# Kernel optimization log

Hardware: AMD Instinct MI355X
Metric: run time of the kernel (lower is better)

## Reference

```python
import jax, jax.numpy as jnp
import numpy as np

N_NODES = 50000
N_EDGES = 800000
F_IN = 16
HEADS = 4
CONV_DIMS = [(16, 16), (16, 32), (32, 32), (32, 32), (32, 32), (32, 64)]
LIN_DIMS = [(128, 256), (256, 64), (64, 16), (16, 1)]


def setup_inputs() -> dict:
    key = jax.random.key(0)
    ks = iter(jax.random.split(key, 64))
    inp = {}
    inp["x"] = jax.random.normal(next(ks), (N_NODES, F_IN), dtype=jnp.float32)
    inp["edge_index"] = jax.random.randint(next(ks), (2, N_EDGES), 0, N_NODES, dtype=jnp.int32)
    for i, (ci, co) in enumerate(CONV_DIMS, 1):
        inp[f"W{i}"] = jax.random.normal(next(ks), (ci, HEADS * co), dtype=jnp.float32) * (1.0 / np.sqrt(ci))
        inp[f"U{i}"] = jax.random.normal(next(ks), (ci, HEADS), dtype=jnp.float32) * (1.0 / np.sqrt(ci))
        inp[f"c{i}"] = jnp.zeros((HEADS,), jnp.float32)
        inp[f"b{i}"] = jnp.zeros((co,), jnp.float32)
    for i, d in zip((1, 2, 3), (32, 32, 64)):
        inp[f"g{i}"] = jnp.ones((d,), jnp.float32)
        inp[f"be{i}"] = jnp.zeros((d,), jnp.float32)
    for name, (ci, co) in zip(("1", "2", "3", "o"), LIN_DIMS):
        inp[f"lw{name}"] = jax.random.normal(next(ks), (ci, co), dtype=jnp.float32) * (1.0 / np.sqrt(ci))
        inp[f"lb{name}"] = jnp.zeros((co,), jnp.float32)
    return inp


def _feast(x, src, dst, W, U, c, b):
    # FeaStConv (PyG): q = softmax_h(U^T (x_j - x_i) + c); out_i = mean_j sum_h q_h * (W_h x_j) + b
    n = x.shape[0]
    out_ch = W.shape[1] // HEADS
    q = jax.nn.softmax((x[src] - x[dst]) @ U + c, axis=-1)            # [E, H]
    xw = (x @ W).reshape(n, HEADS, out_ch)                            # [N, H, O]
    msg = jnp.einsum('eho,eh->eo', xw[src], q)                        # [E, O]
    s = jax.ops.segment_sum(msg, dst, num_segments=n)
    cnt = jax.ops.segment_sum(jnp.ones((src.shape[0], 1), msg.dtype), dst, num_segments=n)
    return s / jnp.maximum(cnt, 1.0) + b


def _bn(x, g, b, eps=1e-5):
    # training-mode BatchNorm over the node dimension
    m = x.mean(0)
    v = x.var(0)
    return (x - m) * jax.lax.rsqrt(v + eps) * g + b


def _forward(x, edge_index, convs, bns, lins):
    # FeaStConv adds self-loops by default
    loops = jnp.arange(x.shape[0], dtype=edge_index.dtype)
    src = jnp.concatenate([edge_index[0], loops])
    dst = jnp.concatenate([edge_index[1], loops])
    h = jax.nn.relu(_feast(x, src, dst, *convs[0]))
    x1 = _bn(jax.nn.relu(_feast(h, src, dst, *convs[1])), *bns[0])
    x2 = jax.nn.relu(_feast(x1, src, dst, *convs[2]))
    x2 = _bn(jax.nn.relu(_feast(x2, src, dst, *convs[3])), *bns[1])
    x3 = jax.nn.relu(_feast(x2, src, dst, *convs[4]))
    x3 = _bn(jax.nn.relu(_feast(x3, src, dst, *convs[5])), *bns[2])
    z = jax.nn.relu(jnp.concatenate([x1, x2, x3], axis=1))            # [N, 128]
    (lw1, lb1), (lw2, lb2), (lw3, lb3), (lwo, lbo) = lins
    z = jax.nn.relu(z @ lw1 + lb1)
    z = jax.nn.relu(z @ lw2 + lb2)
    z = jax.nn.relu(z @ lw3 + lb3)
    return jax.nn.sigmoid(z @ lwo + lbo)                              # [N, 1]


def reference(x, edge_index, W1, U1, c1, b1, W2, U2, c2, b2, W3, U3, c3, b3, W4, U4, c4, b4, W5, U5, c5, b5, W6, U6, c6, b6, g1, be1, g2, be2, g3, be3, lw1, lb1, lw2, lb2, lw3, lb3, lwo, lbo):
    convs = [(W1, U1, c1, b1), (W2, U2, c2, b2), (W3, U3, c3, b3), (W4, U4, c4, b4), (W5, U5, c5, b5), (W6, U6, c6, b6)]
    bns = [(g1, be1), (g2, be2), (g3, be3)]
    lins = [(lw1, lb1), (lw2, lb2), (lw3, lb3), (lwo, lbo)]
    return _forward(x, edge_index, convs, bns, lins)
```

## Files before the change

kernel.cpp:

```cpp
#include <hip/hip_runtime.h>

constexpr int NN = 50000;
constexpr int NE = 800000;
constexpr int SNB = (NN + 255) / 256;

typedef _Float16 h8 __attribute__((ext_vector_type(8)));
typedef _Float16 h4v __attribute__((ext_vector_type(4)));
typedef float f32x4 __attribute__((ext_vector_type(4)));

__global__ void hist_kernel(const int* __restrict__ dst, int* __restrict__ deg) {
    int e = blockIdx.x * blockDim.x + threadIdx.x;
    if (e < NE) atomicAdd(&deg[dst[e]], 1);
}

__global__ __launch_bounds__(256) void scan_bsum_kernel(const int* __restrict__ deg,
                                                        int* __restrict__ bsum) {
    int i = blockIdx.x * 256 + threadIdx.x;
    int v = (i < NN) ? deg[i] : 0;
#pragma unroll
    for (int off = 32; off > 0; off >>= 1) v += __shfl_xor(v, off);
    __shared__ int ws[4];
    if ((threadIdx.x & 63) == 0) ws[threadIdx.x >> 6] = v;
    __syncthreads();
    if (threadIdx.x == 0) bsum[blockIdx.x] = ws[0] + ws[1] + ws[2] + ws[3];
}

__global__ __launch_bounds__(256) void scan_tops_kernel(const int* __restrict__ bsum,
                                                        int* __restrict__ bpre) {
    int tid = threadIdx.x;
    int v = (tid < SNB) ? bsum[tid] : 0;
    int lane = tid & 63, wid = tid >> 6;
    int x = v;
#pragma unroll
    for (int off = 1; off < 64; off <<= 1) {
        int y = __shfl_up(x, off, 64);
        if (lane >= off) x += y;
    }
    __shared__ int wsum[4];
    if (lane == 63) wsum[wid] = x;
    __syncthreads();
    int wpre = 0;
    for (int w = 0; w < wid; w++) wpre += wsum[w];
    if (tid < SNB) bpre[tid] = wpre + x - v;
    if (tid == 0) bpre[SNB] = wsum[0] + wsum[1] + wsum[2] + wsum[3];
}

__global__ __launch_bounds__(256) void scan_final_kernel(const int* __restrict__ deg,
                                                         const int* __restrict__ bpre,
                                                         int* __restrict__ row_ptr,
                                                         int* __restrict__ fillc) {
    int i = blockIdx.x * 256 + threadIdx.x;
    int v = (i < NN) ? deg[i] : 0;
    int lane = threadIdx.x & 63, wid = threadIdx.x >> 6;
    int x = v;
#pragma unroll
    for (int off = 1; off < 64; off <<= 1) {
        int y = __shfl_up(x, off, 64);
        if (lane >= off) x += y;
    }
    __shared__ int wsum[4];
    if (lane == 63) wsum[wid] = x;
    __syncthreads();
    int wpre = 0;
    for (int w = 0; w < wid; w++) wpre += wsum[w];
    int ex = bpre[blockIdx.x] + wpre + x - v;
    if (i < NN) { row_ptr[i] = ex; fillc[i] = ex; }
    if (i == 0) row_ptr[NN] = bpre[SNB];
}

__global__ void fill_kernel(const int* __restrict__ src, const int* __restrict__ dst,
                            int* __restrict__ fillc, int2* __restrict__ col2) {
    int e = blockIdx.x * blockDim.x + threadIdx.x;
    if (e < NE) {
        int d = dst[e];
        int k = atomicAdd(&fillc[d], 1);
        col2[k] = make_int2(src[e], d);
    }
}

template <int CI>
__global__ __launch_bounds__(256) void prep_kernel(const float* __restrict__ x,
                                                   const float* __restrict__ U,
                                                   _Float16* __restrict__ xh,
                                                   float* __restrict__ t) {
    __shared__ float Us[CI * 4];
    for (int i = threadIdx.x; i < CI * 4; i += 256) Us[i] = U[i];
    __syncthreads();
    int n = blockIdx.x * 256 + threadIdx.x;
    if (n >= NN) return;
    float xr[CI];
    const float4* xv = reinterpret_cast<const float4*>(x + (size_t)n * CI);
#pragma unroll
    for (int q = 0; q < CI / 4; q++) {
        float4 v = xv[q];
        xr[4 * q + 0] = v.x; xr[4 * q + 1] = v.y; xr[4 * q + 2] = v.z; xr[4 * q + 3] = v.w;
    }
    h8* xo = reinterpret_cast<h8*>(xh + (size_t)n * CI);
#pragma unroll
    for (int q = 0; q < CI / 8; q++) {
        h8 hv;
#pragma unroll
        for (int u = 0; u < 8; u++) hv[u] = (_Float16)xr[8 * q + u];
        xo[q] = hv;
    }
    float a0 = 0.f, a1 = 0.f, a2 = 0.f, a3 = 0.f;
#pragma unroll
    for (int k = 0; k < CI; k++) {
        float xk = xr[k];
        a0 = fmaf(xk, Us[k * 4 + 0], a0); a1 = fmaf(xk, Us[k * 4 + 1], a1);
        a2 = fmaf(xk, Us[k * 4 + 2], a2); a3 = fmaf(xk, Us[k * 4 + 3], a3);
    }
    reinterpret_cast<float4*>(t)[n] = make_float4(a0, a1, a2, a3);
}

template <int CO>
__global__ __launch_bounds__(256) void tU_kernel(const _Float16* __restrict__ xh,
                                                 const float* __restrict__ U,
                                                 float* __restrict__ t) {
    __shared__ float Us[CO * 4];
    for (int i = threadIdx.x; i < CO * 4; i += 256) Us[i] = U[i];
    __syncthreads();
    int n = blockIdx.x * 256 + threadIdx.x;
    if (n >= NN) return;
    const h8* xp = reinterpret_cast<const h8*>(xh + (size_t)n * CO);
    float t0 = 0.f, t1 = 0.f, t2 = 0.f, t3 = 0.f;
#pragma unroll
    for (int q8 = 0; q8 < CO / 8; q8++) {
        h8 v = xp[q8];
#pragma unroll
        for (int u = 0; u < 8; u++) {
            float r = (float)v[u];
            const float* us = &Us[(q8 * 8 + u) * 4];
            t0 = fmaf(r, us[0], t0); t1 = fmaf(r, us[1], t1);
            t2 = fmaf(r, us[2], t2); t3 = fmaf(r, us[3], t3);
        }
    }
    reinterpret_cast<float4*>(t)[n] = make_float4(t0, t1, t2, t3);
}

__global__ __launch_bounds__(256) void edgeq_kernel(const int2* __restrict__ col2,
                                                    const float* __restrict__ t,
                                                    const float* __restrict__ cvec,
                                                    h4v* __restrict__ qbuf) {
    int k = blockIdx.x * 256 + threadIdx.x;
    if (k >= NE) return;
    int2 sd = col2[k];
    float4 ts = reinterpret_cast<const float4*>(t)[sd.x];
    float4 td = reinterpret_cast<const float4*>(t)[sd.y];
    float4 cv = *reinterpret_cast<const float4*>(cvec);
    float d0 = ts.x - td.x + cv.x, d1 = ts.y - td.y + cv.y;
    float d2 = ts.z - td.z + cv.z, d3 = ts.w - td.w + cv.w;
    float mm = fmaxf(fmaxf(d0, d1), fmaxf(d2, d3));
    float q0 = __expf(d0 - mm), q1 = __expf(d1 - mm);
    float q2 = __expf(d2 - mm), q3 = __expf(d3 - mm);
    float is = 1.f / (q0 + q1 + q2 + q3);
    h4v q;
    q[0] = (_Float16)(q0 * is); q[1] = (_Float16)(q1 * is);
    q[2] = (_Float16)(q2 * is); q[3] = (_Float16)(q3 * is);
    qbuf[k] = q;
}

template <int CI>
__global__ __launch_bounds__(256) void aggC_kernel(const _Float16* __restrict__ xh,
                                                   const h4v* __restrict__ qbuf,
                                                   const float* __restrict__ cvec,
                                                   const int* __restrict__ row_ptr,
                                                   const int2* __restrict__ col2,
                                                   _Float16* __restrict__ y) {
    constexpr int SLOTS = 128 / CI;
    __shared__ float part[2][CI * 4];
    int tid = threadIdx.x;
    int half = tid >> 7;
    int lt = tid & 127;
    int n = blockIdx.x * 2 + half;
    int ch = lt & (CI - 1);
    int slot = lt / CI;
    float4 cv = *reinterpret_cast<const float4*>(cvec);
    float a0 = 0.f, a1 = 0.f, a2 = 0.f, a3 = 0.f;
    if (slot == 0) {
        float m = fmaxf(fmaxf(cv.x, cv.y), fmaxf(cv.z, cv.w));
        float s0 = __expf(cv.x - m), s1 = __expf(cv.y - m),
              s2 = __expf(cv.z - m), s3 = __expf(cv.w - m);
        float sinv = 1.f / (s0 + s1 + s2 + s3);
        float xself = (float)xh[(size_t)n * CI + ch];
        a0 = s0 * sinv * xself; a1 = s1 * sinv * xself;
        a2 = s2 * sinv * xself; a3 = s3 * sinv * xself;
    }
    int beg = row_ptr[n], end = row_ptr[n + 1];
#pragma unroll 2
    for (int e = beg + slot; e < end; e += SLOTS) {
        int s = col2[e].x;
        h4v q = qbuf[e];
        float xv = (float)xh[(size_t)s * CI + ch];
        a0 = fmaf((float)q[0], xv, a0); a1 = fmaf((float)q[1], xv, a1);
        a2 = fmaf((float)q[2], xv, a2); a3 = fmaf((float)q[3], xv, a3);
    }
#pragma unroll
    for (int off = 32; off >= CI; off >>= 1) {
        a0 += __shfl_xor(a0, off); a1 += __shfl_xor(a1, off);
        a2 += __shfl_xor(a2, off); a3 += __shfl_xor(a3, off);
    }
    if (lt >= 64 && lt < 64 + CI) {
        part[half][ch * 4 + 0] = a0; part[half][ch * 4 + 1] = a1;
        part[half][ch * 4 + 2] = a2; part[half][ch * 4 + 3] = a3;
    }
    __syncthreads();
    if (lt < CI) {
        a0 += part[half][ch * 4 + 0]; a1 += part[half][ch * 4 + 1];
        a2 += part[half][ch * 4 + 2]; a3 += part[half][ch * 4 + 3];
        float sc = 1.f / (float)(end - beg + 1);
        _Float16* yo = y + (size_t)n * 4 * CI + ch;
        yo[0]      = (_Float16)(a0 * sc);
        yo[CI]     = (_Float16)(a1 * sc);
        yo[2 * CI] = (_Float16)(a2 * sc);
        yo[3 * CI] = (_Float16)(a3 * sc);
    }
}

template <int K, int CO, int COB, bool STACKED, bool OUT16>
__global__ __launch_bounds__(256) void mfma_dense_kernel(const _Float16* __restrict__ A,
                                                         const float* __restrict__ W,
                                                         const float* __restrict__ bias,
                                                         void* __restrict__ outp) {
    constexpr int KS = K / 16;
    constexpr int OT = COB / 16;
    constexpr int CIc = K / 4;
    __shared__ _Float16 Bf[OT * KS * 64 * 4];
    __shared__ float bS[COB];
    int o0 = blockIdx.y * COB;
    for (int idx = threadIdx.x; idx < OT * KS * 64; idx += 256) {
        int lane = idx & 63;
        int ks = (idx >> 6) % KS;
        int ot = idx / (64 * KS);
        int o = o0 + ot * 16 + (lane & 15);
        int kb = ks * 16 + (lane >> 4) * 4;
        h4v v;
#pragma unroll
        for (int j = 0; j < 4; j++) {
            int k = kb + j;
            float wv;
            if constexpr (STACKED) wv = W[(k % CIc) * (4 * CO) + (k / CIc) * CO + o];
            else                   wv = W[k * CO + o];
            v[j] = (_Float16)wv;
        }
        *reinterpret_cast<h4v*>(&Bf[idx * 4]) = v;
    }
    for (int i = threadIdx.x; i < COB; i += 256) bS[i] = bias[o0 + i];
    __syncthreads();
    int wid = threadIdx.x >> 6, lane = threadIdx.x & 63;
    int row_in = lane & 15;
    int kgrp = lane >> 4;
    for (int mt = blockIdx.x * 4 + wid; mt < NN / 16; mt += gridDim.x * 4) {
        int m0 = mt * 16;
        f32x4 acc[OT];
#pragma unroll
        for (int t = 0; t < OT; t++) acc[t] = {0.f, 0.f, 0.f, 0.f};
        const _Float16* Ab = A + (size_t)(m0 + row_in) * K + kgrp * 4;
#pragma unroll
        for (int ks = 0; ks < KS; ks++) {
            h4v af = *reinterpret_cast<const h4v*>(Ab + ks * 16);
#pragma unroll
            for (int t = 0; t < OT; t++) {
                h4v bf = *reinterpret_cast<const h4v*>(&Bf[((t * KS + ks) * 64 + lane) * 4]);
                acc[t] = __builtin_amdgcn_mfma_f32_16x16x16f16(af, bf, acc[t], 0, 0, 0);
            }
        }
        int orow0 = m0 + kgrp * 4;
#pragma unroll
        for (int t = 0; t < OT; t++) {
            int col = o0 + t * 16 + row_in;
            float b = bS[t * 16 + row_in];
#pragma unroll
            for (int i = 0; i < 4; i++) {
                float v = fmaxf(acc[t][i] + b, 0.f);
                if constexpr (OUT16)
                    ((_Float16*)outp)[(size_t)(orow0 + i) * CO + col] = (_Float16)v;
                else
                    ((float*)outp)[(size_t)(orow0 + i) * CO + col] = v;
            }
        }
    }
}

template <int C>
__global__ __launch_bounds__(256) void bn_reduce_kernel(const float* __restrict__ a,
                                                        float* __restrict__ stats) {
    constexpr int R = 256 / C;
    int cidx = threadIdx.x % C;
    int r = threadIdx.x / C;
    float s = 0.f, s2 = 0.f;
    for (int n = blockIdx.x * R + r; n < NN; n += gridDim.x * R) {
        float v = a[(size_t)n * C + cidx];
        s += v; s2 = fmaf(v, v, s2);
    }
    __shared__ float ls[256], ls2[256];
    ls[threadIdx.x] = s; ls2[threadIdx.x] = s2;
    __syncthreads();
    for (int off = 128; off >= C; off >>= 1) {
        if (threadIdx.x < off) {
            ls[threadIdx.x] += ls[threadIdx.x + off];
            ls2[threadIdx.x] += ls2[threadIdx.x + off];
        }
        __syncthreads();
    }
    if (threadIdx.x < C) {
        atomicAdd(&stats[cidx], ls[threadIdx.x]);
        atomicAdd(&stats[C + cidx], ls2[threadIdx.x]);
    }
}

template <int C>
__global__ __launch_bounds__(256) void bn_norm_prep_kernel(const float* __restrict__ a,
                                                           const float* __restrict__ stats,
                                                           const float* __restrict__ g,
                                                           const float* __restrict__ be,
                                                           const float* __restrict__ U,
                                                           _Float16* __restrict__ xh,
                                                           float* __restrict__ t,
                                                           _Float16* __restrict__ zh,
                                                           int zoff) {
    __shared__ float mS[C], sS[C], beS[C], Us[C * 4];
    if (threadIdx.x < C) {
        int c = threadIdx.x;
        float mean = stats[c] * (1.f / NN);
        float var = stats[C + c] * (1.f / NN) - mean * mean;
        mS[c] = mean;
        sS[c] = rsqrtf(fmaxf(var, 0.f) + 1e-5f) * g[c];
        beS[c] = be[c];
    }
    for (int i = threadIdx.x; i < C * 4; i += 256) Us[i] = U[i];
    __syncthreads();
    int n = blockIdx.x * 256 + threadIdx.x;
    if (n >= NN) return;
    const float4* ap = reinterpret_cast<const float4*>(a + (size_t)n * C);
    h8* xo = reinterpret_cast<h8*>(xh + (size_t)n * C);
    h8* zo = reinterpret_cast<h8*>(zh + (size_t)n * 128 + zoff);
    float t0 = 0.f, t1 = 0.f, t2 = 0.f, t3 = 0.f;
#pragma unroll
    for (int q8 = 0; q8 < C / 8; q8++) {
        h8 hv, zv;
#pragma unroll
        for (int q4 = 0; q4 < 2; q4++) {
            int c4 = q8 * 2 + q4;
            float4 v = ap[c4];
            float r0 = (v.x - mS[c4 * 4 + 0]) * sS[c4 * 4 + 0] + beS[c4 * 4 + 0];
            float r1 = (v.y - mS[c4 * 4 + 1]) * sS[c4 * 4 + 1] + beS[c4 * 4 + 1];
            float r2 = (v.z - mS[c4 * 4 + 2]) * sS[c4 * 4 + 2] + beS[c4 * 4 + 2];
            float r3 = (v.w - mS[c4 * 4 + 3]) * sS[c4 * 4 + 3] + beS[c4 * 4 + 3];
            hv[q4 * 4 + 0] = (_Float16)r0; hv[q4 * 4 + 1] = (_Float16)r1;
            hv[q4 * 4 + 2] = (_Float16)r2; hv[q4 * 4 + 3] = (_Float16)r3;
            zv[q4 * 4 + 0] = (_Float16)fmaxf(r0, 0.f); zv[q4 * 4 + 1] = (_Float16)fmaxf(r1, 0.f);
            zv[q4 * 4 + 2] = (_Float16)fmaxf(r2, 0.f); zv[q4 * 4 + 3] = (_Float16)fmaxf(r3, 0.f);
            const float* us;
            us = &Us[(c4 * 4 + 0) * 4];
            t0 = fmaf(r0, us[0], t0); t1 = fmaf(r0, us[1], t1); t2 = fmaf(r0, us[2], t2); t3 = fmaf(r0, us[3], t3);
            us = &Us[(c4 * 4 + 1) * 4];
            t0 = fmaf(r1, us[0], t0); t1 = fmaf(r1, us[1], t1); t2 = fmaf(r1, us[2], t2); t3 = fmaf(r1, us[3], t3);
            us = &Us[(c4 * 4 + 2) * 4];
            t0 = fmaf(r2, us[0], t0); t1 = fmaf(r2, us[1], t1); t2 = fmaf(r2, us[2], t2); t3 = fmaf(r2, us[3], t3);
            us = &Us[(c4 * 4 + 3) * 4];
            t0 = fmaf(r3, us[0], t0); t1 = fmaf(r3, us[1], t1); t2 = fmaf(r3, us[2], t2); t3 = fmaf(r3, us[3], t3);
        }
        xo[q8] = hv;
        zo[q8] = zv;
    }
    reinterpret_cast<float4*>(t)[n] = make_float4(t0, t1, t2, t3);
}

template <int C>
__global__ __launch_bounds__(256) void bn_norm_z_kernel(const float* __restrict__ a,
                                                        const float* __restrict__ stats,
                                                        const float* __restrict__ g,
                                                        const float* __restrict__ be,
                                                        _Float16* __restrict__ zh,
                                                        int zoff) {
    __shared__ float mS[C], sS[C], beS[C];
    if (threadIdx.x < C) {
        int c = threadIdx.x;
        float mean = stats[c] * (1.f / NN);
        float var = stats[C + c] * (1.f / NN) - mean * mean;
        mS[c] = mean;
        sS[c] = rsqrtf(fmaxf(var, 0.f) + 1e-5f) * g[c];
        beS[c] = be[c];
    }
    __syncthreads();
    int n = blockIdx.x * 256 + threadIdx.x;
    if (n >= NN) return;
    const float4* ap = reinterpret_cast<const float4*>(a + (size_t)n * C);
    h8* zo = reinterpret_cast<h8*>(zh + (size_t)n * 128 + zoff);
#pragma unroll
    for (int q8 = 0; q8 < C / 8; q8++) {
        h8 zv;
#pragma unroll
        for (int q4 = 0; q4 < 2; q4++) {
            int c4 = q8 * 2 + q4;
            float4 v = ap[c4];
            zv[q4 * 4 + 0] = (_Float16)fmaxf((v.x - mS[c4 * 4 + 0]) * sS[c4 * 4 + 0] + beS[c4 * 4 + 0], 0.f);
            zv[q4 * 4 + 1] = (_Float16)fmaxf((v.y - mS[c4 * 4 + 1]) * sS[c4 * 4 + 1] + beS[c4 * 4 + 1], 0.f);
            zv[q4 * 4 + 2] = (_Float16)fmaxf((v.z - mS[c4 * 4 + 2]) * sS[c4 * 4 + 2] + beS[c4 * 4 + 2], 0.f);
            zv[q4 * 4 + 3] = (_Float16)fmaxf((v.w - mS[c4 * 4 + 3]) * sS[c4 * 4 + 3] + beS[c4 * 4 + 3], 0.f);
        }
        zo[q8] = zv;
    }
}

__global__ __launch_bounds__(256) void lin3o_kernel(const _Float16* __restrict__ z2,
                                                    const float* __restrict__ lw3,
                                                    const float* __restrict__ lb3,
                                                    const float* __restrict__ lwo,
                                                    const float* __restrict__ lbo,
                                                    float* __restrict__ out) {
    __shared__ float W3s[64 * 16];
    __shared__ float Wos[16];
    __shared__ float b3s[16];
    for (int i = threadIdx.x; i < 64 * 16; i += 256) W3s[i] = lw3[i];
    if (threadIdx.x < 16) { Wos[threadIdx.x] = lwo[threadIdx.x]; b3s[threadIdx.x] = lb3[threadIdx.x]; }
    __syncthreads();
    int n = blockIdx.x * 256 + threadIdx.x;
    if (n >= NN) return;
    float acc[16];
#pragma unroll
    for (int u = 0; u < 16; u++) acc[u] = b3s[u];
    const h8* zp = reinterpret_cast<const h8*>(z2 + (size_t)n * 64);
#pragma unroll
    for (int k8 = 0; k8 < 8; k8++) {
        h8 v = zp[k8];
#pragma unroll
        for (int u = 0; u < 8; u++) {
            float vf = (float)v[u];
            const float* w = &W3s[(k8 * 8 + u) * 16];
#pragma unroll
            for (int o = 0; o < 16; o++) acc[o] = fmaf(vf, w[o], acc[o]);
        }
    }
    float s = lbo[0];
#pragma unroll
    for (int u = 0; u < 16; u++) s = fmaf(fmaxf(acc[u], 0.f), Wos[u], s);
    out[n] = 1.f / (1.f + __expf(-s));
}

extern "C" void kernel_launch(void* const* d_in, const int* in_sizes, int n_in,
                              void* d_out, int out_size, void* d_ws, size_t ws_size,
                              hipStream_t stream) {
    const float* x = (const float*)d_in[0];
    const int* ei = (const int*)d_in[1];
    const int* esrc = ei;
    const int* edst = ei + NE;
    const float* W[6]; const float* U[6]; const float* C[6]; const float* B[6];
    for (int i = 0; i < 6; i++) {
        W[i] = (const float*)d_in[2 + 4 * i];
        U[i] = (const float*)d_in[3 + 4 * i];
        C[i] = (const float*)d_in[4 + 4 * i];
        B[i] = (const float*)d_in[5 + 4 * i];
    }
    const float* g1 = (const float*)d_in[26]; const float* be1 = (const float*)d_in[27];
    const float* g2 = (const float*)d_in[28]; const float* be2 = (const float*)d_in[29];
    const float* g3 = (const float*)d_in[30]; const float* be3 = (const float*)d_in[31];
    const float* lw1 = (const float*)d_in[32]; const float* lb1 = (const float*)d_in[33];
    const float* lw2 = (const float*)d_in[34]; const float* lb2 = (const float*)d_in[35];
    const float* lw3 = (const float*)d_in[36]; const float* lb3 = (const float*)d_in[37];
    const float* lwo = (const float*)d_in[38]; const float* lbo = (const float*)d_in[39];

    char* w = (char*)d_ws;
    size_t o = 0;
    auto take = [&](size_t bytes) -> char* {
        char* p = w + o;
        o = (o + bytes + 255) & ~(size_t)255;
        return p;
    };
    int* deg = (int*)take((size_t)NN * 4);
    float* stats = (float*)take(3 * 256 * 4);
    size_t zero_bytes = o;
    int* fillc = (int*)take((size_t)NN * 4);
    int* row_ptr = (int*)take((size_t)(NN + 1) * 4);
    int* bsum = (int*)take((size_t)(SNB + 1) * 4);
    int* bpre = (int*)take((size_t)(SNB + 1) * 4);
    int2* col2 = (int2*)take((size_t)NE * 8);
    h4v* qbuf = (h4v*)take((size_t)NE * 8);
    float* t = (float*)take((size_t)NN * 4 * 4);
    _Float16* xh = (_Float16*)take((size_t)NN * 32 * 2);
    char* A = take((size_t)NN * 256 * 2);
    _Float16* y = (_Float16*)A;
    _Float16* z1h = (_Float16*)A;
    _Float16* zh = (_Float16*)take((size_t)NN * 128 * 2);
    float* tmp = (float*)take((size_t)NN * 64 * 4);
    _Float16* z2h = (_Float16*)tmp;
    float* st0 = stats, *st1 = stats + 256, *st2 = stats + 512;

    hipMemsetAsync(d_ws, 0, zero_bytes, stream);

    const int EB = (NE + 255) / 256;
    const int NB = (NN + 255) / 256;
    const int GB = 250;

    hist_kernel<<<EB, 256, 0, stream>>>(edst, deg);
    scan_bsum_kernel<<<SNB, 256, 0, stream>>>(deg, bsum);
    scan_tops_kernel<<<1, 256, 0, stream>>>(bsum, bpre);
    scan_final_kernel<<<SNB, 256, 0, stream>>>(deg, bpre, row_ptr, fillc);
    fill_kernel<<<EB, 256, 0, stream>>>(esrc, edst, fillc, col2);

    prep_kernel<16><<<NB, 256, 0, stream>>>(x, U[0], xh, t);
    edgeq_kernel<<<EB, 256, 0, stream>>>(col2, t, C[0], qbuf);
    aggC_kernel<16><<<NN / 2, 256, 0, stream>>>(xh, qbuf, C[0], row_ptr, col2, y);
    mfma_dense_kernel<64, 16, 16, true, true><<<dim3(GB, 1), 256, 0, stream>>>(y, W[0], B[0], xh);
    tU_kernel<16><<<NB, 256, 0, stream>>>(xh, U[1], t);
    edgeq_kernel<<<EB, 256, 0, stream>>>(col2, t, C[1], qbuf);
    aggC_kernel<16><<<NN / 2, 256, 0, stream>>>(xh, qbuf, C[1], row_ptr, col2, y);
    mfma_dense_kernel<64, 32, 32, true, false><<<dim3(GB, 1), 256, 0, stream>>>(y, W[1], B[1], tmp);
    bn_reduce_kernel<32><<<256, 256, 0, stream>>>(tmp, st0);
    bn_norm_prep_kernel<32><<<NB, 256, 0, stream>>>(tmp, st0, g1, be1, U[2], xh, t, zh, 0);
    edgeq_kernel<<<EB, 256, 0, stream>>>(col2, t, C[2], qbuf);
    aggC_kernel<32><<<NN / 2, 256, 0, stream>>>(xh, qbuf, C[2], row_ptr, col2, y);
    mfma_dense_kernel<128, 32, 32, true, true><<<dim3(GB, 1), 256, 0, stream>>>(y, W[2], B[2], xh);
    tU_kernel<32><<<NB, 256, 0, stream>>>(xh, U[3], t);
    edgeq_kernel<<<EB, 256, 0, stream>>>(col2, t, C[3], qbuf);
    aggC_kernel<32><<<NN / 2, 256, 0, stream>>>(xh, qbuf, C[3], row_ptr, col2, y);
    mfma_dense_kernel<128, 32, 32, true, false><<<dim3(GB, 1), 256, 0, stream>>>(y, W[3], B[3], tmp);
    bn_reduce_kernel<32><<<256, 256, 0, stream>>>(tmp, st1);
    bn_norm_prep_kernel<32><<<NB, 256, 0, stream>>>(tmp, st1, g2, be2, U[4], xh, t, zh, 32);
    edgeq_kernel<<<EB, 256, 0, stream>>>(col2, t, C[4], qbuf);
    aggC_kernel<32><<<NN / 2, 256, 0, stream>>>(xh, qbuf, C[4], row_ptr, col2, y);
    mfma_dense_kernel<128, 32, 32, true, true><<<dim3(GB, 1), 256, 0, stream>>>(y, W[4], B[4], xh);
    tU_kernel<32><<<NB, 256, 0, stream>>>(xh, U[5], t);
    edgeq_kernel<<<EB, 256, 0, stream>>>(col2, t, C[5], qbuf);
    aggC_kernel<32><<<NN / 2, 256, 0, stream>>>(xh, qbuf, C[5], row_ptr, col2, y);
    mfma_dense_kernel<128, 64, 64, true, false><<<dim3(GB, 1), 256, 0, stream>>>(y, W[5], B[5], tmp);
    bn_reduce_kernel<64><<<256, 256, 0, stream>>>(tmp, st2);
    bn_norm_z_kernel<64><<<NB, 256, 0, stream>>>(tmp, st2, g3, be3, zh, 64);

    mfma_dense_kernel<128, 256, 64, false, true><<<dim3(GB, 4), 256, 0, stream>>>(zh, lw1, lb1, z1h);
    mfma_dense_kernel<256, 64, 64, false, true><<<dim3(GB, 1), 256, 0, stream>>>(z1h, lw2, lb2, z2h);
    lin3o_kernel<<<NB, 256, 0, stream>>>(z2h, lw3, lb3, lwo, lbo, (float*)d_out);
}
```

Before: 653.0 us.

## Fuse U-projection into dense epilogue and make edge softmax CSR node-parallel

Removes the separate tU kernel by computing the per-node head projection t = relu(xW+b)·U inside the MFMA dense kernel epilogue, using a 16-lane shuffle reduction. The edge softmax kernel now walks CSR rows with 16 lanes per node, so the destination's t is loaded once and the edge list only stores source indices (int instead of int2). This halves the column array traffic for both edgeq and aggregation, and the aggregation loop unroll goes from 2 to 4. In exchange the dense epilogue does extra shuffles and register work, and the per-node edge loop may leave lanes idle on low-degree nodes.

```diff
diff --git a/kernel.cpp b/kernel.cpp
--- a/kernel.cpp
+++ b/kernel.cpp
@@ -69,12 +69,12 @@
 }
 
 __global__ void fill_kernel(const int* __restrict__ src, const int* __restrict__ dst,
-                            int* __restrict__ fillc, int2* __restrict__ col2) {
+                            int* __restrict__ fillc, int* __restrict__ col) {
     int e = blockIdx.x * blockDim.x + threadIdx.x;
     if (e < NE) {
         int d = dst[e];
         int k = atomicAdd(&fillc[d], 1);
-        col2[k] = make_int2(src[e], d);
+        col[k] = src[e];
     }
 }
 
@@ -113,51 +113,31 @@
     reinterpret_cast<float4*>(t)[n] = make_float4(a0, a1, a2, a3);
 }
 
-template <int CO>
-__global__ __launch_bounds__(256) void tU_kernel(const _Float16* __restrict__ xh,
-                                                 const float* __restrict__ U,
-                                                 float* __restrict__ t) {
-    __shared__ float Us[CO * 4];
-    for (int i = threadIdx.x; i < CO * 4; i += 256) Us[i] = U[i];
-    __syncthreads();
-    int n = blockIdx.x * 256 + threadIdx.x;
-    if (n >= NN) return;
-    const h8* xp = reinterpret_cast<const h8*>(xh + (size_t)n * CO);
-    float t0 = 0.f, t1 = 0.f, t2 = 0.f, t3 = 0.f;
-#pragma unroll
-    for (int q8 = 0; q8 < CO / 8; q8++) {
-        h8 v = xp[q8];
-#pragma unroll
-        for (int u = 0; u < 8; u++) {
-            float r = (float)v[u];
-            const float* us = &Us[(q8 * 8 + u) * 4];
-            t0 = fmaf(r, us[0], t0); t1 = fmaf(r, us[1], t1);
-            t2 = fmaf(r, us[2], t2); t3 = fmaf(r, us[3], t3);
-        }
-    }
-    reinterpret_cast<float4*>(t)[n] = make_float4(t0, t1, t2, t3);
-}
-
-__global__ __launch_bounds__(256) void edgeq_kernel(const int2* __restrict__ col2,
+__global__ __launch_bounds__(256) void edgeq_kernel(const int* __restrict__ col,
+                                                    const int* __restrict__ row_ptr,
                                                     const float* __restrict__ t,
                                                     const float* __restrict__ cvec,
                                                     h4v* __restrict__ qbuf) {
-    int k = blockIdx.x * 256 + threadIdx.x;
-    if (k >= NE) return;
-    int2 sd = col2[k];
-    float4 ts = reinterpret_cast<const float4*>(t)[sd.x];
-    float4 td = reinterpret_cast<const float4*>(t)[sd.y];
+    int n = blockIdx.x * 16 + (threadIdx.x >> 4);
+    if (n >= NN) return;
+    int l16 = threadIdx.x & 15;
     float4 cv = *reinterpret_cast<const float4*>(cvec);
-    float d0 = ts.x - td.x + cv.x, d1 = ts.y - td.y + cv.y;
-    float d2 = ts.z - td.z + cv.z, d3 = ts.w - td.w + cv.w;
-    float mm = fmaxf(fmaxf(d0, d1), fmaxf(d2, d3));
-    float q0 = __expf(d0 - mm), q1 = __expf(d1 - mm);
-    float q2 = __expf(d2 - mm), q3 = __expf(d3 - mm);
-    float is = 1.f / (q0 + q1 + q2 + q3);
-    h4v q;
-    q[0] = (_Float16)(q0 * is); q[1] = (_Float16)(q1 * is);
-    q[2] = (_Float16)(q2 * is); q[3] = (_Float16)(q3 * is);
-    qbuf[k] = q;
+    float4 td = reinterpret_cast<const float4*>(t)[n];
+    float b0 = cv.x - td.x, b1 = cv.y - td.y, b2 = cv.z - td.z, b3 = cv.w - td.w;
+    int beg = row_ptr[n], end = row_ptr[n + 1];
+    for (int e = beg + l16; e < end; e += 16) {
+        int s = col[e];
+        float4 ts = reinterpret_cast<const float4*>(t)[s];
+        float d0 = ts.x + b0, d1 = ts.y + b1, d2 = ts.z + b2, d3 = ts.w + b3;
+        float mm = fmaxf(fmaxf(d0, d1), fmaxf(d2, d3));
+        float q0 = __expf(d0 - mm), q1 = __expf(d1 - mm);
+        float q2 = __expf(d2 - mm), q3 = __expf(d3 - mm);
+        float is = 1.f / (q0 + q1 + q2 + q3);
+        h4v q;
+        q[0] = (_Float16)(q0 * is); q[1] = (_Float16)(q1 * is);
+        q[2] = (_Float16)(q2 * is); q[3] = (_Float16)(q3 * is);
+        qbuf[e] = q;
+    }
 }
 
 template <int CI>
@@ -165,7 +145,7 @@
                                                    const h4v* __restrict__ qbuf,
                                                    const float* __restrict__ cvec,
                                                    const int* __restrict__ row_ptr,
-                                                   const int2* __restrict__ col2,
+                                                   const int* __restrict__ col,
                                                    _Float16* __restrict__ y) {
     constexpr int SLOTS = 128 / CI;
     __shared__ float part[2][CI * 4];
@@ -187,9 +167,9 @@
         a2 = s2 * sinv * xself; a3 = s3 * sinv * xself;
     }
     int beg = row_ptr[n], end = row_ptr[n + 1];
-#pragma unroll 2
+#pragma unroll 4
     for (int e = beg + slot; e < end; e += SLOTS) {
-        int s = col2[e].x;
+        int s = col[e];
         h4v q = qbuf[e];
         float xv = (float)xh[(size_t)s * CI + ch];
         a0 = fmaf((float)q[0], xv, a0); a1 = fmaf((float)q[1], xv, a1);
@@ -217,16 +197,19 @@
     }
 }
 
-template <int K, int CO, int COB, bool STACKED, bool OUT16>
+template <int K, int CO, int COB, bool STACKED, bool OUT16, bool TPREP>
 __global__ __launch_bounds__(256) void mfma_dense_kernel(const _Float16* __restrict__ A,
                                                          const float* __restrict__ W,
                                                          const float* __restrict__ bias,
-                                                         void* __restrict__ outp) {
+                                                         const float* __restrict__ U,
+                                                         void* __restrict__ outp,
+                                                         float* __restrict__ tout) {
     constexpr int KS = K / 16;
     constexpr int OT = COB / 16;
     constexpr int CIc = K / 4;
     __shared__ _Float16 Bf[OT * KS * 64 * 4];
     __shared__ float bS[COB];
+    __shared__ float Us[TPREP ? CO * 4 : 4];
     int o0 = blockIdx.y * COB;
     for (int idx = threadIdx.x; idx < OT * KS * 64; idx += 256) {
         int lane = idx & 63;
@@ -246,6 +229,9 @@
         *reinterpret_cast<h4v*>(&Bf[idx * 4]) = v;
     }
     for (int i = threadIdx.x; i < COB; i += 256) bS[i] = bias[o0 + i];
+    if constexpr (TPREP) {
+        for (int i = threadIdx.x; i < CO * 4; i += 256) Us[i] = U[i];
+    }
     __syncthreads();
     int wid = threadIdx.x >> 6, lane = threadIdx.x & 63;
     int row_in = lane & 15;
@@ -268,16 +254,42 @@
         int orow0 = m0 + kgrp * 4;
 #pragma unroll
         for (int t = 0; t < OT; t++) {
-            int col = o0 + t * 16 + row_in;
+            int colo = o0 + t * 16 + row_in;
             float b = bS[t * 16 + row_in];
 #pragma unroll
             for (int i = 0; i < 4; i++) {
                 float v = fmaxf(acc[t][i] + b, 0.f);
+                acc[t][i] = v;
                 if constexpr (OUT16)
-                    ((_Float16*)outp)[(size_t)(orow0 + i) * CO + col] = (_Float16)v;
+                    ((_Float16*)outp)[(size_t)(orow0 + i) * CO + colo] = (_Float16)v;
                 else
-                    ((float*)outp)[(size_t)(orow0 + i) * CO + col] = v;
+                    ((float*)outp)[(size_t)(orow0 + i) * CO + colo] = v;
             }
+        }
+        if constexpr (TPREP) {
+            float p[4][4];
+#pragma unroll
+            for (int i = 0; i < 4; i++)
+#pragma unroll
+                for (int h = 0; h < 4; h++) p[i][h] = 0.f;
+#pragma unroll
+            for (int tt = 0; tt < OT; tt++) {
+                const float* ur = &Us[(tt * 16 + row_in) * 4];
+#pragma unroll
+                for (int i = 0; i < 4; i++) {
+                    float v = acc[tt][i];
+#pragma unroll
+                    for (int h = 0; h < 4; h++) p[i][h] = fmaf(v, ur[h], p[i][h]);
+                }
+            }
+#pragma unroll
+            for (int mask = 1; mask < 16; mask <<= 1) {
+#pragma unroll
+                for (int i = 0; i < 4; i++)
+#pragma unroll
+                    for (int h = 0; h < 4; h++) p[i][h] += __shfl_xor(p[i][h], mask);
+            }
+            tout[(size_t)(orow0 + (row_in >> 2)) * 4 + (row_in & 3)] = p[row_in >> 2][row_in & 3];
         }
     }
 }
@@ -475,7 +487,7 @@
     int* row_ptr = (int*)take((size_t)(NN + 1) * 4);
     int* bsum = (int*)take((size_t)(SNB + 1) * 4);
     int* bpre = (int*)take((size_t)(SNB + 1) * 4);
-    int2* col2 = (int2*)take((size_t)NE * 8);
+    int* colA = (int*)take((size_t)NE * 4);
     h4v* qbuf = (h4v*)take((size_t)NE * 8);
     float* t = (float*)take((size_t)NN * 4 * 4);
     _Float16* xh = (_Float16*)take((size_t)NN * 32 * 2);
@@ -491,44 +503,42 @@
 
     const int EB = (NE + 255) / 256;
     const int NB = (NN + 255) / 256;
+    const int QB = (NN + 15) / 16;
     const int GB = 250;
 
     hist_kernel<<<EB, 256, 0, stream>>>(edst, deg);
     scan_bsum_kernel<<<SNB, 256, 0, stream>>>(deg, bsum);
     scan_tops_kernel<<<1, 256, 0, stream>>>(bsum, bpre);
     scan_final_kernel<<<SNB, 256, 0, stream>>>(deg, bpre, row_ptr, fillc);
-    fill_kernel<<<EB, 256, 0, stream>>>(esrc, edst, fillc, col2);
+    fill_kernel<<<EB, 256, 0, stream>>>(esrc, edst, fillc, colA);
 
     prep_kernel<16><<<NB, 256, 0, stream>>>(x, U[0], xh, t);
-    edgeq_kernel<<<EB, 256, 0, stream>>>(col2, t, C[0], qbuf);
-    aggC_kernel<16><<<NN / 2, 256, 0, stream>>>(xh, qbuf, C[0], row_ptr, col2, y);
-    mfma_dense_kernel<64, 16, 16, true, true><<<dim3(GB, 1), 256, 0, stream>>>(y, W[0], B[0], xh);
-    tU_kernel<16><<<NB, 256, 0, stream>>>(xh, U[1], t);
-    edgeq_kernel<<<EB, 256, 0, stream>>>(col2, t, C[1], qbuf);
-    aggC_kernel<16><<<NN / 2, 256, 0, stream>>>(xh, qbuf, C[1], row_ptr, col2, y);
-    mfma_dense_kernel<64, 32, 32, true, false><<<dim3(GB, 1), 256, 0, stream>>>(y, W[1], B[1], tmp);
+    edgeq_kernel<<<QB, 256, 0, stream>>>(colA, row_ptr, t, C[0], qbuf);
+    aggC_kernel<16><<<NN / 2, 256, 0, stream>>>(xh, qbuf, C[0], row_ptr, colA, y);
+    mfma_dense_kernel<64, 16, 16, true, true, true><<<dim3(GB, 1), 256, 0, stream>>>(y, W[0], B[0], U[1], xh, t);
+    edgeq_kernel<<<QB, 256, 0, stream>>>(colA, row_ptr, t, C[1], qbuf);
+    aggC_kernel<16><<<NN / 2, 256, 0, stream>>>(xh, qbuf, C[1], row_ptr, colA, y);
+    mfma_dense_kernel<64, 32, 32, true, false, false><<<dim3(GB, 1), 256, 0, stream>>>(y, W[1], B[1], nullptr, tmp, nullptr);
     bn_reduce_kernel<32><<<256, 256, 0, stream>>>(tmp, st0);
     bn_norm_prep_kernel<32><<<NB, 256, 0, stream>>>(tmp, st0, g1, be1, U[2], xh, t, zh, 0);
-    edgeq_kernel<<<EB, 256, 0, stream>>>(col2, t, C[2], qbuf);
-    aggC_kernel<32><<<NN / 2, 256, 0, stream>>>(xh, qbuf, C[2], row_ptr, col2, y);
-    mfma_dense_kernel<128, 32, 32, true, true><<<dim3(GB, 1), 256, 0, stream>>>(y, W[2], B[2], xh);
-    tU_kernel<32><<<NB, 256, 0, stream>>>(xh, U[3], t);
-    edgeq_kernel<<<EB, 256, 0, stream>>>(col2, t, C[3], qbuf);
-    aggC_kernel<32><<<NN / 2, 256, 0, stream>>>(xh, qbuf, C[3], row_ptr, col2, y);
-    mfma_dense_kernel<128, 32, 32, true, false><<<dim3(GB, 1), 256, 0, stream>>>(y, W[3], B[3], tmp);
+    edgeq_kernel<<<QB, 256, 0, stream>>>(colA, row_ptr, t, C[2], qbuf);
+    aggC_kernel<32><<<NN / 2, 256, 0, stream>>>(xh, qbuf, C[2], row_ptr, colA, y);
+    mfma_dense_kernel<128, 32, 32, true, true, true><<<dim3(GB, 1), 256, 0, stream>>>(y, W[2], B[2], U[3], xh, t);
+    edgeq_kernel<<<QB, 256, 0, stream>>>(colA, row_ptr, t, C[3], qbuf);
+    aggC_kernel<32><<<NN / 2, 256, 0, stream>>>(xh, qbuf, C[3], row_ptr, colA, y);
+    mfma_dense_kernel<128, 32, 32, true, false, false><<<dim3(GB, 1), 256, 0, stream>>>(y, W[3], B[3], nullptr, tmp, nullptr);
     bn_reduce_kernel<32><<<256, 256, 0, stream>>>(tmp, st1);
     bn_norm_prep_kernel<32><<<NB, 256, 0, stream>>>(tmp, st1, g2, be2, U[4], xh, t, zh, 32);
-    edgeq_kernel<<<EB, 256, 0, stream>>>(col2, t, C[4], qbuf);
-    aggC_kernel<32><<<NN / 2, 256, 0, stream>>>(xh, qbuf, C[4], row_ptr, col2, y);
-    mfma_dense_kernel<128, 32, 32, true, true><<<dim3(GB, 1), 256, 0, stream>>>(y, W[4], B[4], xh);
-    tU_kernel<32><<<NB, 256, 0, stream>>>(xh, U[5], t);
-    edgeq_kernel<<<EB, 256, 0, stream>>>(col2, t, C[5], qbuf);
-    aggC_kernel<32><<<NN / 2, 256, 0, stream>>>(xh, qbuf, C[5], row_ptr, col2, y);
-    mfma_dense_kernel<128, 64, 64, true, false><<<dim3(GB, 1), 256, 0, stream>>>(y, W[5], B[5], tmp);
+    edgeq_kernel<<<QB, 256, 0, stream>>>(colA, row_ptr, t, C[4], qbuf);
+    aggC_kernel<32><<<NN / 2, 256, 0, stream>>>(xh, qbuf, C[4], row_ptr, colA, y);
+    mfma_dense_kernel<128, 32, 32, true, true, true><<<dim3(GB, 1), 256, 0, stream>>>(y, W[4], B[4], U[5], xh, t);
+    edgeq_kernel<<<QB, 256, 0, stream>>>(colA, row_ptr, t, C[5], qbuf);
+    aggC_kernel<32><<<NN / 2, 256, 0, stream>>>(xh, qbuf, C[5], row_ptr, colA, y);
+    mfma_dense_kernel<128, 64, 64, true, false, false><<<dim3(GB, 1), 256, 0, stream>>>(y, W[5], B[5], nullptr, tmp, nullptr);
     bn_reduce_kernel<64><<<256, 256, 0, stream>>>(tmp, st2);
     bn_norm_z_kernel<64><<<NB, 256, 0, stream>>>(tmp, st2, g3, be3, zh, 64);
 
-    mfma_dense_kernel<128, 256, 64, false, true><<<dim3(GB, 4), 256, 0, stream>>>(zh, lw1, lb1, z1h);
-    mfma_dense_kernel<256, 64, 64, false, true><<<dim3(GB, 1), 256, 0, stream>>>(z1h, lw2, lb2, z2h);
+    mfma_dense_kernel<128, 256, 64, false, true, false><<<dim3(GB, 4), 256, 0, stream>>>(zh, lw1, lb1, nullptr, z1h, nullptr);
+    mfma_dense_kernel<256, 64, 64, false, true, false><<<dim3(GB, 1), 256, 0, stream>>>(z1h, lw2, lb2, nullptr, z2h, nullptr);
     lin3o_kernel<<<NB, 256, 0, stream>>>(z2h, lw3, lb3, lwo, lbo, (float*)d_out);
 }
```

Result: slower. 695.1 us (+6.4%).
